# Kernel tuning notes

Hardware: AMD Instinct MI355X
Metric: run time of the kernel (lower is better)

Reference implementation:

```python
import jax, jax.numpy as jnp
import numpy as np

IN_F, OUT_F, K = 64, 64, 3
EPS = 1e-05
C_EQ = 1.0 / np.sqrt(IN_F * K * K)  # equalized-lr constant


def setup_inputs() -> dict:
    key = jax.random.key(0)
    k1, k2 = jax.random.split(key)
    x = jax.random.normal(k1, (16, IN_F, 256, 256), dtype=jnp.float32)
    weight = jax.random.normal(k2, (OUT_F, IN_F, K, K), dtype=jnp.float32)
    return {"x": x, "weight": weight}


def reference(x, weight):
    # Equalized-lr scaling
    w = weight * jnp.asarray(C_EQ, dtype=weight.dtype)  # [O, I, K, K]
    # Demodulation: per-output-channel rsqrt of sum of squares over (I, K, K).
    # With no style modulation the factor is identical for every sample, so the
    # original groups=batch conv is exactly a plain conv2d with these weights.
    sigma_inv = jax.lax.rsqrt(jnp.sum(w * w, axis=(1, 2, 3), keepdims=True) + EPS)
    w = w * sigma_inv  # [O, I, K, K]
    out = jax.lax.conv_general_dilated(
        x, w,
        window_strides=(1, 1),
        padding=[(1, 1), (1, 1)],  # (k-1)//2 = 1
        dimension_numbers=("NCHW", "OIHW", "NCHW"),
    )
    return out  # [B, O, H, W]
```

## Files before the change

### kernel.cpp

```cpp
#include <hip/hip_runtime.h>
#include <hip/hip_bf16.h>
#include <math.h>

#define BATCH 16
#define ICH 64
#define OCH 64
#define HH 256
#define WW 256
#define HW 65536
#define EPS 1e-5f
#define C_EQ (1.0f / 24.0f)

typedef __attribute__((ext_vector_type(8))) short short8;
typedef __attribute__((ext_vector_type(4))) float floatx4;

#define AFRAG_BYTES 73728
#define XT_PIX 258
#define XT_ROWB (XT_PIX * 128)
#define XT_IMGB ((size_t)XT_PIX * XT_PIX * 128)
#define WS_NEEDED (AFRAG_BYTES + (size_t)BATCH * XT_IMGB)

#define AS1 __attribute__((address_space(1)))
#define AS3 __attribute__((address_space(3)))

static __device__ __forceinline__ unsigned short f2bf(float v) {
    __hip_bfloat16 b = __float2bfloat16(v);
    return *reinterpret_cast<unsigned short*>(&b);
}
static __device__ __forceinline__ unsigned int pk2(float a, float b) {
    return (unsigned int)f2bf(a) | ((unsigned int)f2bf(b) << 16);
}

__global__ void weight_prep_kernel(const float* __restrict__ wgt,
                                   unsigned int* __restrict__ wsout)
{
    const int tid = threadIdx.x;
    const int oc  = blockIdx.x * 16 + (tid >> 2);
    const int q   = tid & 3;
    const float* wb = wgt + ((size_t)oc * 64 + q * 16) * 9;

    float s = 0.f;
    #pragma unroll 4
    for (int i = 0; i < 36; ++i) {
        const float4 v = reinterpret_cast<const float4*>(wb)[i];
        s += v.x*v.x + v.y*v.y + v.z*v.z + v.w*v.w;
    }
    s += __shfl_xor(s, 1, 64);
    s += __shfl_xor(s, 2, 64);
    const float sc = C_EQ * rsqrtf(s * (C_EQ * C_EQ) + EPS);

    const int h = q >> 1;
    #pragma unroll
    for (int s2 = 0; s2 < 2; ++s2) {
        const int G = (q & 1) * 2 + s2;
        #pragma unroll
        for (int jp = 0; jp < 4; ++jp) {
            const float* r0 = wb + (8 * s2 + 2 * jp) * 9;
            const float* r1 = r0 + 9;
            #pragma unroll
            for (int t = 0; t < 9; ++t) {
                const unsigned int d = (unsigned)f2bf(r0[t] * sc)
                                     | ((unsigned)f2bf(r1[t] * sc) << 16);
                wsout[(((h * 9 + t) * 64 + oc) * 4 + G) * 4 + jp] = d;
            }
        }
    }
}

__global__ __launch_bounds__(256, 8) void transpose_pad_kernel(
    const float* __restrict__ x, char* __restrict__ xT)
{
    const int tid  = threadIdx.x;
    const int lane = tid & 63;
    const int wvv  = tid >> 6;
    const int cb = blockIdx.x, hh = blockIdx.y, b = blockIdx.z;
    char* rowbase = xT + (size_t)b * XT_IMGB + (size_t)hh * XT_ROWB;
    const uint4 z4 = make_uint4(0u, 0u, 0u, 0u);

    if (hh == 0 || hh == XT_PIX - 1) {
        char* base = rowbase + (size_t)(cb * 64 + 1) * 128;
        *reinterpret_cast<uint4*>(base + tid * 32)      = z4;
        *reinterpret_cast<uint4*>(base + tid * 32 + 16) = z4;
        if (cb == 0 && tid < 8)
            *reinterpret_cast<uint4*>(rowbase + tid * 16) = z4;
        if (cb == 3 && tid >= 8 && tid < 16)
            *reinterpret_cast<uint4*>(rowbase + (size_t)257 * 128 + (tid - 8) * 16) = z4;
        return;
    }
    if (cb == 0 && tid < 8)
        *reinterpret_cast<uint4*>(rowbase + tid * 16) = z4;
    if (cb == 3 && tid >= 8 && tid < 16)
        *reinterpret_cast<uint4*>(rowbase + (size_t)257 * 128 + (tid - 8) * 16) = z4;

    __shared__ float lds[64 * 65];
    const int h = hh - 1;
    const float* xrow = x + (size_t)b * ICH * HW + (size_t)h * WW + cb * 64;
    float v[16];
    #pragma unroll
    for (int i = 0; i < 16; ++i)
        v[i] = xrow[(size_t)(i * 4 + wvv) * HW + lane];
    #pragma unroll
    for (int i = 0; i < 16; ++i)
        lds[lane * 65 + i * 4 + wvv] = v[i];
    __syncthreads();

    const int col = tid >> 2;
    const int g   = tid & 3;
    const float* lp = &lds[col * 65];
    char* dst = rowbase + (size_t)(cb * 64 + col + 1) * 128;
    #pragma unroll
    for (int r = 0; r < 2; ++r) {
        const int ich = r * 32 + g * 8;
        uint4 dw;
        dw.x = pk2(lp[ich + 0], lp[ich + 1]);
        dw.y = pk2(lp[ich + 2], lp[ich + 3]);
        dw.z = pk2(lp[ich + 4], lp[ich + 5]);
        dw.w = pk2(lp[ich + 6], lp[ich + 7]);
        *reinterpret_cast<uint4*>(dst + r * 64 + g * 16) = dw;
    }
}

__global__ __launch_bounds__(256, 3) void conv_mfma_lds(
    const char* __restrict__ ws, float* __restrict__ out)
{
    __shared__ __align__(16) char lx[6 * 8448];

    const int tid  = threadIdx.x;
    const int lane = tid & 63;
    const int wv   = tid >> 6;
    const int n_l  = lane & 15;
    const int G_l  = lane >> 4;

    const int bid = blockIdx.x;
    const int wg  = (bid & 7) * 512 + (bid >> 3);
    const int b   = wg >> 8;
    const int ry  = (wg >> 2) & 63;
    const int cb  = wg & 3;
    const int gc0 = cb * 64;
    const int gr0 = ry * 4;

    const char* xTb = ws + AFRAG_BYTES + (size_t)b * XT_IMGB;
    const unsigned abase = (n_l << 6) + (G_l << 4);

    short8 A0[4], A1[4];
#define LOADA4(Ab, kc) { _Pragma("unroll") for (int og = 0; og < 4; ++og) \
    Ab[og] = *reinterpret_cast<const short8*>(ws + ((kc) << 12) + (og << 10) + abase); }
    LOADA4(A0, 0); LOADA4(A1, 3);

    const unsigned laneoff = ((unsigned)(lane >> 3) << 7)
                           + ((unsigned)((lane & 7) ^ (lane >> 3)) << 4);
    #pragma unroll
    for (int t = 0; t < 14; ++t) {
        const int i = wv + 4 * t;
        if (i >= 54) break;
        const int row = i / 9;
        const int k   = i - row * 9;
        const char* src = xTb + (size_t)(gr0 + row) * XT_ROWB
                        + ((unsigned)gc0 << 7) + ((unsigned)k << 10) + laneoff;
        if (k < 8 || lane < 16)
            __builtin_amdgcn_global_load_lds(
                (const AS1 void*)src,
                (AS3 void*)&lx[row * 8448 + (k << 10)], 16, 0, 0);
    }

    int boff[3][2];
    #pragma unroll
    for (int kw = 0; kw < 3; ++kw) {
        const int px = (wv << 4) + n_l + kw;
        #pragma unroll
        for (int h = 0; h < 2; ++h)
            boff[kw][h] = (px << 7) + ((((h << 2) | G_l) ^ (px & 7)) << 4);
    }

    floatx4 acc[4][4];
    #pragma unroll
    for (int og = 0; og < 4; ++og)
        #pragma unroll
        for (int fr = 0; fr < 4; ++fr) acc[og][fr] = (floatx4){0.f, 0.f, 0.f, 0.f};

    __syncthreads();

    uint4 B[6];
#define LOADB6(kw, h) { _Pragma("unroll") for (int j = 0; j < 6; ++j) \
    B[j] = *reinterpret_cast<const uint4*>(&lx[j * 8448 + boff[kw][h]]); }
#define TAPH(Ab, kh) { _Pragma("unroll") for (int og = 0; og < 4; ++og) { \
    _Pragma("unroll") for (int fr = 0; fr < 4; ++fr) \
      acc[og][fr] = __builtin_amdgcn_mfma_f32_16x16x32_bf16( \
          Ab[og], __builtin_bit_cast(short8, B[fr + (kh)]), acc[og][fr], 0, 0, 0); } }

    LOADB6(0, 0);
    TAPH(A0, 0); LOADA4(A0, 6);
    TAPH(A1, 1); LOADA4(A1, 1);
    TAPH(A0, 2); LOADA4(A0, 4);
    LOADB6(1, 0);
    TAPH(A1, 0); LOADA4(A1, 7);
    TAPH(A0, 1); LOADA4(A0, 2);
    TAPH(A1, 2); LOADA4(A1, 5);
    LOADB6(2, 0);
    TAPH(A0, 0); LOADA4(A0, 8);
    TAPH(A1, 1); LOADA4(A1, 9);
    TAPH(A0, 2); LOADA4(A0, 12);
    LOADB6(0, 1);
    TAPH(A1, 0); LOADA4(A1, 15);
    TAPH(A0, 1); LOADA4(A0, 10);
    TAPH(A1, 2); LOADA4(A1, 13);
    LOADB6(1, 1);
    TAPH(A0, 0); LOADA4(A0, 16);
    TAPH(A1, 1); LOADA4(A1, 11);
    TAPH(A0, 2); LOADA4(A0, 14);
    LOADB6(2, 1);
    TAPH(A1, 0); LOADA4(A1, 17);
    TAPH(A0, 1);
    TAPH(A1, 2);
#undef LOADB6
#undef LOADA4
#undef TAPH

    float* lf = (float*)lx;
    const int colw = (wv << 4) + n_l;
    #pragma unroll
    for (int half = 0; half < 2; ++half) {
        __syncthreads();
        #pragma unroll
        for (int og2 = 0; og2 < 2; ++og2) {
            const int og = half * 2 + og2;
            #pragma unroll
            for (int fr = 0; fr < 4; ++fr) {
                const int rbase = (og2 * 16 + (G_l << 2)) * 4 + fr;
                #pragma unroll
                for (int ri = 0; ri < 4; ++ri)
                    lf[(rbase + ri * 4) * 68 + colw] = acc[og][fr][ri];
            }
        }
        __syncthreads();
        const int q = tid & 15;
        #pragma unroll
        for (int j = 0; j < 8; ++j) {
            const int row = (tid >> 4) + (j << 4);
            const int ocl = row >> 2, fr = row & 3;
            const float4 v = *reinterpret_cast<const float4*>(&lf[row * 68 + (q << 2)]);
            float* op = out + ((size_t)b * OCH + half * 32 + ocl) * HW
                            + (size_t)(gr0 + fr) * WW + gc0 + (q << 2);
            *reinterpret_cast<float4*>(op) = v;
        }
    }
}

#define TR 4
#define TC 64
#define XROWS 6
#define XCOLS 66
#define XPIXB 64
#define XROWB (XCOLS * XPIXB)
#define XHALFB (XROWS * XROWB)
#define LDS_BYTES (2 * XHALFB)

__global__ __launch_bounds__(256, 2) void conv_mfma_fallback(
    const float* __restrict__ x,
    const unsigned int* __restrict__ wfrag,
    float* __restrict__ out)
{
    __shared__ __align__(16) char lds[LDS_BYTES];
    const int tid  = threadIdx.x;
    const int lane = tid & 63;
    const int wv   = tid >> 6;
    const int n_l  = lane & 15;
    const int G_l  = lane >> 4;

    short8 afrag[18];
    {
        const int oc_l = (wv << 4) + n_l;
        const char* wsb = (const char*)wfrag;
        #pragma unroll
        for (int kc = 0; kc < 18; ++kc)
            afrag[kc] = *reinterpret_cast<const short8*>(
                wsb + (((kc * 64 + oc_l) * 4 + G_l) << 4));
    }

    const int gr0 = blockIdx.y * TR;
    const int gc0 = blockIdx.x * TC;
    const int b   = blockIdx.z;
    const float* xb = x + (size_t)b * ICH * HW;

    for (int p = wv; p < 48; p += 4) {
        const int h  = p / 24;
        const int pr = (p % 24) >> 2;
        const int G  = p & 3;
        const int gr = gr0 - 1 + pr;
        const int icb = h * 32 + G * 8;
        const bool rok = ((unsigned)gr < (unsigned)HH);
        {
            const float* src = xb + (size_t)icb * HW + (size_t)gr * WW + gc0 + lane;
            float v[8];
            #pragma unroll
            for (int qq = 0; qq < 8; ++qq) v[qq] = rok ? src[(size_t)qq * HW] : 0.f;
            const int pc = lane + 1;
            const int addr = h*XHALFB + pr*XROWB + pc*XPIXB + ((G ^ ((pc >> 1) & 3)) << 4);
            uint4 w4; w4.x = pk2(v[0], v[1]); w4.y = pk2(v[2], v[3]);
            w4.z = pk2(v[4], v[5]); w4.w = pk2(v[6], v[7]);
            *reinterpret_cast<uint4*>(&lds[addr]) = w4;
        }
        if (lane < 2) {
            const int pc = lane * 65;
            const int gc = gc0 - 1 + pc;
            const bool ok = rok && ((unsigned)gc < (unsigned)WW);
            const float* src = xb + (size_t)icb * HW + (size_t)gr * WW + gc;
            float v[8];
            #pragma unroll
            for (int qq = 0; qq < 8; ++qq) v[qq] = ok ? src[(size_t)qq * HW] : 0.f;
            const int addr = h*XHALFB + pr*XROWB + pc*XPIXB + ((G ^ ((pc >> 1) & 3)) << 4);
            uint4 w4; w4.x = pk2(v[0], v[1]); w4.y = pk2(v[2], v[3]);
            w4.z = pk2(v[4], v[5]); w4.w = pk2(v[6], v[7]);
            *reinterpret_cast<uint4*>(&lds[addr]) = w4;
        }
    }
    __syncthreads();

    int colp[4][3];
    #pragma unroll
    for (int cbq = 0; cbq < 4; ++cbq)
        #pragma unroll
        for (int kw = 0; kw < 3; ++kw) {
            const int pcv = cbq * 16 + n_l + kw;
            colp[cbq][kw] = pcv * XPIXB + ((G_l ^ ((pcv >> 1) & 3)) << 4);
        }

    floatx4 acc[16];
    #pragma unroll
    for (int f = 0; f < 16; ++f) acc[f] = (floatx4){0.f, 0.f, 0.f, 0.f};

    #pragma unroll
    for (int kc = 0; kc < 18; ++kc) {
        const int h = kc / 9, tap = kc % 9;
        const int kh = tap / 3, kw = tap % 3;
        #pragma unroll
        for (int f = 0; f < 16; ++f) {
            const int fr = f >> 2, cbq = f & 3;
            const short8 bfrag = *reinterpret_cast<const short8*>(
                &lds[h*XHALFB + (fr + kh)*XROWB + colp[cbq][kw]]);
            acc[f] = __builtin_amdgcn_mfma_f32_16x16x32_bf16(afrag[kc], bfrag, acc[f], 0, 0, 0);
        }
    }

    float* ob = out + ((size_t)(b*OCH + (wv << 4) + (G_l << 2)) * HW)
                    + (size_t)gr0 * WW + gc0 + n_l;
    #pragma unroll
    for (int f = 0; f < 16; ++f) {
        const int fr = f >> 2, cbq = f & 3;
        #pragma unroll
        for (int ri = 0; ri < 4; ++ri)
            ob[(size_t)ri * HW + fr * WW + cbq * 16] = acc[f][ri];
    }
}

extern "C" void kernel_launch(void* const* d_in, const int* in_sizes, int n_in,
                              void* d_out, int out_size, void* d_ws, size_t ws_size,
                              hipStream_t stream) {
    const float* x = (const float*)d_in[0];
    const float* w = (const float*)d_in[1];
    float* out = (float*)d_out;
    unsigned int* wsf = (unsigned int*)d_ws;

    weight_prep_kernel<<<dim3(4), 64, 0, stream>>>(w, wsf);

    if (ws_size >= WS_NEEDED) {
        char* xT = (char*)d_ws + AFRAG_BYTES;
        transpose_pad_kernel<<<dim3(4, XT_PIX, BATCH), 256, 0, stream>>>(x, xT);
        conv_mfma_lds<<<dim3(4096), 256, 0, stream>>>((const char*)d_ws, out);
    } else {
        conv_mfma_fallback<<<dim3(4, 64, BATCH), 256, 0, stream>>>(x, wsf, out);
    }
}
```

Measured before the change: 246.4 us.

## Split conv into single-wave workgroups to drop block-wide barriers

Each workgroup is now one 64-lane wave computing a 4x16 output tile, with 16384 blocks instead of 4096 four-wave blocks. Each wave stages its own input halo into a smaller LDS buffer and waits with s_waitcnt instead of __syncthreads. The output transpose through LDS also needs no barriers. The intent is to remove barrier stalls and let waves run independently. The cost is extra halo reads (18 columns per 16 instead of 66 per 64) and a per-wave 17-float LDS row stride, which leaves the float4 reads misaligned.

After: 286.2 us. +16.2%, slower.

```diff
diff --git a/kernel.cpp b/kernel.cpp
--- a/kernel.cpp
+++ b/kernel.cpp
@@ -120,24 +120,22 @@
     }
 }
 
-__global__ __launch_bounds__(256, 3) void conv_mfma_lds(
+__global__ __launch_bounds__(64, 3) void conv_mfma_wave(
     const char* __restrict__ ws, float* __restrict__ out)
 {
-    __shared__ __align__(16) char lx[6 * 8448];
-
-    const int tid  = threadIdx.x;
-    const int lane = tid & 63;
-    const int wv   = tid >> 6;
+    __shared__ __align__(16) char lx[6 * 2304];
+
+    const int lane = threadIdx.x;
     const int n_l  = lane & 15;
     const int G_l  = lane >> 4;
 
     const int bid = blockIdx.x;
-    const int wg  = (bid & 7) * 512 + (bid >> 3);
-    const int b   = wg >> 8;
-    const int ry  = (wg >> 2) & 63;
-    const int cb  = wg & 3;
-    const int gc0 = cb * 64;
+    const int wg  = (bid & 7) * 2048 + (bid >> 3);
+    const int b   = wg >> 10;
+    const int ry  = (wg >> 4) & 63;
+    const int cw  = wg & 15;
     const int gr0 = ry * 4;
+    const int gc0 = cw * 16;
 
     const char* xTb = ws + AFRAG_BYTES + (size_t)b * XT_IMGB;
     const unsigned abase = (n_l << 6) + (G_l << 4);
@@ -150,23 +148,21 @@
     const unsigned laneoff = ((unsigned)(lane >> 3) << 7)
                            + ((unsigned)((lane & 7) ^ (lane >> 3)) << 4);
     #pragma unroll
-    for (int t = 0; t < 14; ++t) {
-        const int i = wv + 4 * t;
-        if (i >= 54) break;
-        const int row = i / 9;
-        const int k   = i - row * 9;
-        const char* src = xTb + (size_t)(gr0 + row) * XT_ROWB
-                        + ((unsigned)gc0 << 7) + ((unsigned)k << 10) + laneoff;
-        if (k < 8 || lane < 16)
-            __builtin_amdgcn_global_load_lds(
-                (const AS1 void*)src,
-                (AS3 void*)&lx[row * 8448 + (k << 10)], 16, 0, 0);
+    for (int row = 0; row < 6; ++row) {
+        const char* srow = xTb + (size_t)(gr0 + row) * XT_ROWB + ((unsigned)gc0 << 7);
+        __builtin_amdgcn_global_load_lds((const AS1 void*)(srow + laneoff),
+                                         (AS3 void*)&lx[row * 2304], 16, 0, 0);
+        __builtin_amdgcn_global_load_lds((const AS1 void*)(srow + 1024 + laneoff),
+                                         (AS3 void*)&lx[row * 2304 + 1024], 16, 0, 0);
+        if (lane < 16)
+            __builtin_amdgcn_global_load_lds((const AS1 void*)(srow + 2048 + laneoff),
+                                             (AS3 void*)&lx[row * 2304 + 2048], 16, 0, 0);
     }
 
     int boff[3][2];
     #pragma unroll
     for (int kw = 0; kw < 3; ++kw) {
-        const int px = (wv << 4) + n_l + kw;
+        const int px = n_l + kw;
         #pragma unroll
         for (int h = 0; h < 2; ++h)
             boff[kw][h] = (px << 7) + ((((h << 2) | G_l) ^ (px & 7)) << 4);
@@ -178,11 +174,11 @@
         #pragma unroll
         for (int fr = 0; fr < 4; ++fr) acc[og][fr] = (floatx4){0.f, 0.f, 0.f, 0.f};
 
-    __syncthreads();
+    asm volatile("s_waitcnt vmcnt(0)" ::: "memory");
 
     uint4 B[6];
 #define LOADB6(kw, h) { _Pragma("unroll") for (int j = 0; j < 6; ++j) \
-    B[j] = *reinterpret_cast<const uint4*>(&lx[j * 8448 + boff[kw][h]]); }
+    B[j] = *reinterpret_cast<const uint4*>(&lx[j * 2304 + boff[kw][h]]); }
 #define TAPH(Ab, kh) { _Pragma("unroll") for (int og = 0; og < 4; ++og) { \
     _Pragma("unroll") for (int fr = 0; fr < 4; ++fr) \
       acc[og][fr] = __builtin_amdgcn_mfma_f32_16x16x32_bf16( \
@@ -217,30 +213,24 @@
 #undef TAPH
 
     float* lf = (float*)lx;
-    const int colw = (wv << 4) + n_l;
     #pragma unroll
     for (int half = 0; half < 2; ++half) {
-        __syncthreads();
         #pragma unroll
         for (int og2 = 0; og2 < 2; ++og2) {
             const int og = half * 2 + og2;
             #pragma unroll
-            for (int fr = 0; fr < 4; ++fr) {
-                const int rbase = (og2 * 16 + (G_l << 2)) * 4 + fr;
+            for (int fr = 0; fr < 4; ++fr)
                 #pragma unroll
                 for (int ri = 0; ri < 4; ++ri)
-                    lf[(rbase + ri * 4) * 68 + colw] = acc[og][fr][ri];
-            }
-        }
-        __syncthreads();
-        const int q = tid & 15;
+                    lf[((og2 * 16 + (G_l << 2) + ri) * 4 + fr) * 17 + n_l] = acc[og][fr][ri];
+        }
         #pragma unroll
         for (int j = 0; j < 8; ++j) {
-            const int row = (tid >> 4) + (j << 4);
+            const int row = (lane >> 2) + (j << 4);
             const int ocl = row >> 2, fr = row & 3;
-            const float4 v = *reinterpret_cast<const float4*>(&lf[row * 68 + (q << 2)]);
+            const float4 v = *reinterpret_cast<const float4*>(&lf[row * 17 + (lane & 3) * 4]);
             float* op = out + ((size_t)b * OCH + half * 32 + ocl) * HW
-                            + (size_t)(gr0 + fr) * WW + gc0 + (q << 2);
+                            + (size_t)(gr0 + fr) * WW + gc0 + (lane & 3) * 4;
             *reinterpret_cast<float4*>(op) = v;
         }
     }
@@ -366,7 +356,7 @@
     if (ws_size >= WS_NEEDED) {
         char* xT = (char*)d_ws + AFRAG_BYTES;
         transpose_pad_kernel<<<dim3(4, XT_PIX, BATCH), 256, 0, stream>>>(x, xT);
-        conv_mfma_lds<<<dim3(4096), 256, 0, stream>>>((const char*)d_ws, out);
+        conv_mfma_wave<<<dim3(16384), 64, 0, stream>>>((const char*)d_ws, out);
     } else {
         conv_mfma_fallback<<<dim3(4, 64, BATCH), 256, 0, stream>>>(x, wsf, out);
     }
```

## Split output channels across waves and keep all weight fragments in registers

Applied to the files above, without the earlier changes.

Each wave now owns 16 output channels across all 64 columns, so instead of every wave loading all 4 output-channel groups of A, each wave holds its own 18 weight fragments in registers for the whole kernel. B fragments are now read from LDS per column block, which means more LDS reads of the input tile. The change removes the repeated global/L2 weight reloads interleaved with the MFMAs. Launch bounds drop from 3 to 2 blocks per SIMD to make room for the larger register footprint, which may lower occupancy.

New measurement: 215.4 us. 1.14x faster.

```diff
diff --git a/kernel.cpp b/kernel.cpp
--- a/kernel.cpp
+++ b/kernel.cpp
@@ -120,7 +120,7 @@
     }
 }
 
-__global__ __launch_bounds__(256, 3) void conv_mfma_lds(
+__global__ __launch_bounds__(256, 2) void conv_mfma_ogsplit(
     const char* __restrict__ ws, float* __restrict__ out)
 {
     __shared__ __align__(16) char lx[6 * 8448];
@@ -135,17 +135,19 @@
     const int wg  = (bid & 7) * 512 + (bid >> 3);
     const int b   = wg >> 8;
     const int ry  = (wg >> 2) & 63;
-    const int cb  = wg & 3;
-    const int gc0 = cb * 64;
+    const int cbk = wg & 3;
+    const int gc0 = cbk * 64;
     const int gr0 = ry * 4;
 
     const char* xTb = ws + AFRAG_BYTES + (size_t)b * XT_IMGB;
-    const unsigned abase = (n_l << 6) + (G_l << 4);
-
-    short8 A0[4], A1[4];
-#define LOADA4(Ab, kc) { _Pragma("unroll") for (int og = 0; og < 4; ++og) \
-    Ab[og] = *reinterpret_cast<const short8*>(ws + ((kc) << 12) + (og << 10) + abase); }
-    LOADA4(A0, 0); LOADA4(A1, 3);
+
+    short8 A[18];
+    {
+        const unsigned abase = (unsigned)((wv << 10) + (n_l << 6) + (G_l << 4));
+        #pragma unroll
+        for (int kc = 0; kc < 18; ++kc)
+            A[kc] = *reinterpret_cast<const short8*>(ws + (kc << 12) + abase);
+    }
 
     const unsigned laneoff = ((unsigned)(lane >> 3) << 7)
                            + ((unsigned)((lane & 7) ^ (lane >> 3)) << 4);
@@ -163,74 +165,50 @@
                 (AS3 void*)&lx[row * 8448 + (k << 10)], 16, 0, 0);
     }
 
-    int boff[3][2];
-    #pragma unroll
-    for (int kw = 0; kw < 3; ++kw) {
-        const int px = (wv << 4) + n_l + kw;
-        #pragma unroll
-        for (int h = 0; h < 2; ++h)
-            boff[kw][h] = (px << 7) + ((((h << 2) | G_l) ^ (px & 7)) << 4);
-    }
-
     floatx4 acc[4][4];
     #pragma unroll
-    for (int og = 0; og < 4; ++og)
-        #pragma unroll
-        for (int fr = 0; fr < 4; ++fr) acc[og][fr] = (floatx4){0.f, 0.f, 0.f, 0.f};
+    for (int cb = 0; cb < 4; ++cb)
+        #pragma unroll
+        for (int fr = 0; fr < 4; ++fr) acc[cb][fr] = (floatx4){0.f, 0.f, 0.f, 0.f};
 
     __syncthreads();
 
-    uint4 B[6];
-#define LOADB6(kw, h) { _Pragma("unroll") for (int j = 0; j < 6; ++j) \
-    B[j] = *reinterpret_cast<const uint4*>(&lx[j * 8448 + boff[kw][h]]); }
-#define TAPH(Ab, kh) { _Pragma("unroll") for (int og = 0; og < 4; ++og) { \
-    _Pragma("unroll") for (int fr = 0; fr < 4; ++fr) \
-      acc[og][fr] = __builtin_amdgcn_mfma_f32_16x16x32_bf16( \
-          Ab[og], __builtin_bit_cast(short8, B[fr + (kh)]), acc[og][fr], 0, 0, 0); } }
-
-    LOADB6(0, 0);
-    TAPH(A0, 0); LOADA4(A0, 6);
-    TAPH(A1, 1); LOADA4(A1, 1);
-    TAPH(A0, 2); LOADA4(A0, 4);
-    LOADB6(1, 0);
-    TAPH(A1, 0); LOADA4(A1, 7);
-    TAPH(A0, 1); LOADA4(A0, 2);
-    TAPH(A1, 2); LOADA4(A1, 5);
-    LOADB6(2, 0);
-    TAPH(A0, 0); LOADA4(A0, 8);
-    TAPH(A1, 1); LOADA4(A1, 9);
-    TAPH(A0, 2); LOADA4(A0, 12);
-    LOADB6(0, 1);
-    TAPH(A1, 0); LOADA4(A1, 15);
-    TAPH(A0, 1); LOADA4(A0, 10);
-    TAPH(A1, 2); LOADA4(A1, 13);
-    LOADB6(1, 1);
-    TAPH(A0, 0); LOADA4(A0, 16);
-    TAPH(A1, 1); LOADA4(A1, 11);
-    TAPH(A0, 2); LOADA4(A0, 14);
-    LOADB6(2, 1);
-    TAPH(A1, 0); LOADA4(A1, 17);
-    TAPH(A0, 1);
-    TAPH(A1, 2);
-#undef LOADB6
-#undef LOADA4
-#undef TAPH
+    #pragma unroll
+    for (int ph = 0; ph < 6; ++ph) {
+        const int kw = ph % 3, h = ph / 3;
+        #pragma unroll
+        for (int cb = 0; cb < 4; ++cb) {
+            const int px = cb * 16 + n_l + kw;
+            const int bo = (px << 7) + ((((h << 2) | G_l) ^ (px & 7)) << 4);
+            uint4 B[6];
+            #pragma unroll
+            for (int j = 0; j < 6; ++j)
+                B[j] = *reinterpret_cast<const uint4*>(&lx[j * 8448 + bo]);
+            #pragma unroll
+            for (int kh = 0; kh < 3; ++kh) {
+                const short8 a = A[h * 9 + kh * 3 + kw];
+                #pragma unroll
+                for (int fr = 0; fr < 4; ++fr)
+                    acc[cb][fr] = __builtin_amdgcn_mfma_f32_16x16x32_bf16(
+                        a, __builtin_bit_cast(short8, B[fr + kh]), acc[cb][fr], 0, 0, 0);
+            }
+        }
+    }
 
     float* lf = (float*)lx;
-    const int colw = (wv << 4) + n_l;
     #pragma unroll
     for (int half = 0; half < 2; ++half) {
         __syncthreads();
-        #pragma unroll
-        for (int og2 = 0; og2 < 2; ++og2) {
-            const int og = half * 2 + og2;
-            #pragma unroll
-            for (int fr = 0; fr < 4; ++fr) {
-                const int rbase = (og2 * 16 + (G_l << 2)) * 4 + fr;
+        if ((wv >> 1) == half) {
+            const int ocl16 = (wv & 1) << 4;
+            #pragma unroll
+            for (int cb = 0; cb < 4; ++cb)
                 #pragma unroll
-                for (int ri = 0; ri < 4; ++ri)
-                    lf[(rbase + ri * 4) * 68 + colw] = acc[og][fr][ri];
-            }
+                for (int fr = 0; fr < 4; ++fr)
+                    #pragma unroll
+                    for (int ri = 0; ri < 4; ++ri)
+                        lf[((ocl16 + (G_l << 2) + ri) * 4 + fr) * 68 + cb * 16 + n_l]
+                            = acc[cb][fr][ri];
         }
         __syncthreads();
         const int q = tid & 15;
@@ -366,7 +344,7 @@
     if (ws_size >= WS_NEEDED) {
         char* xT = (char*)d_ws + AFRAG_BYTES;
         transpose_pad_kernel<<<dim3(4, XT_PIX, BATCH), 256, 0, stream>>>(x, xT);
-        conv_mfma_lds<<<dim3(4096), 256, 0, stream>>>((const char*)d_ws, out);
+        conv_mfma_ogsplit<<<dim3(4096), 256, 0, stream>>>((const char*)d_ws, out);
     } else {
         conv_mfma_fallback<<<dim3(4, 64, BATCH), 256, 0, stream>>>(x, wsf, out);
     }
```
